# Kernel tuning notes

Hardware: AMD Instinct MI355X
Metric: run time of the kernel (lower is better)

## Reference

```python
import jax, jax.numpy as jnp
import numpy as np

# Haar (db1) filters after the index reversals done in create_wavelet_filter.
_S = np.float32(1.0 / np.sqrt(2.0))
_LO = np.array([_S, _S], np.float32)
_HI = np.array([_S, -_S], np.float32)
# dec[k, i, j]; band order: LL, (hi rows)*lo, lo*(hi cols), HH -> matches torch stack order
_DEC = np.stack([np.outer(_LO, _LO), np.outer(_HI, _LO), np.outer(_LO, _HI), np.outer(_HI, _HI)], 0)
_REC = _DEC  # identical for Haar


def dwt(x):
    # non-overlapping 2x2 stride-2 depthwise conv == blocked einsum
    b, c, h, w = x.shape
    xr = x.reshape(b, c, h // 2, 2, w // 2, 2)
    return jnp.einsum('bcipjq,kpq->bckij', xr, jnp.asarray(_DEC))  # [b,c,4,h/2,w/2]


def idwt(x):
    # stride-2 kernel-2 transposed depthwise conv == blocked einsum
    b, c, _, h, w = x.shape
    y = jnp.einsum('bckij,kpq->bcipjq', x, jnp.asarray(_REC))
    return y.reshape(b, c, 2 * h, 2 * w)


def dwconv3(x, w, bias=None):
    # depthwise 3x3 'same' conv; w: [C,1,3,3]
    c = x.shape[1]
    y = jax.lax.conv_general_dilated(x, w, (1, 1), 'SAME', feature_group_count=c,
                                     dimension_numbers=('NCHW', 'OIHW', 'NCHW'))
    if bias is not None:
        y = y + bias[None, :, None, None]
    return y


def setup_inputs() -> dict:
    key = jax.random.key(0)
    ks = jax.random.split(key, 8)
    B, C, H, W = 16, 64, 256, 256
    inp = {
        'x': jax.random.normal(ks[0], (B, C, H, W), jnp.float32),
        'base_w': jax.random.normal(ks[1], (C, 1, 3, 3), jnp.float32) * 0.1,
        'base_b': jax.random.normal(ks[2], (C,), jnp.float32) * 0.01,
        'base_scale': jnp.ones((1, C, 1, 1), jnp.float32),
        'ww0': jax.random.normal(ks[3], (4 * C, 1, 3, 3), jnp.float32) * 0.1,
        'ww1': jax.random.normal(ks[4], (4 * C, 1, 3, 3), jnp.float32) * 0.1,
        'ww2': jax.random.normal(ks[5], (4 * C, 1, 3, 3), jnp.float32) * 0.1,
        'ws0': jnp.full((1, 4 * C, 1, 1), 0.1, jnp.float32),
        'ws1': jnp.full((1, 4 * C, 1, 1), 0.1, jnp.float32),
        'ws2': jnp.full((1, 4 * C, 1, 1), 0.1, jnp.float32),
        'gamma': jnp.ones((C,), jnp.float32),
        'beta': jnp.zeros((C,), jnp.float32),
    }
    return inp


def reference(x, base_w, base_b, base_scale, ww0, ww1, ww2, ws0, ws1, ws2, gamma, beta):
    wws = [ww0, ww1, ww2]
    wss = [ws0, ws1, ws2]
    levels = 3
    lls, hs = [], []
    cur = x
    # --- WTConv2d: recursive wavelet pyramid (H,W divisible by 2**levels, no odd-pad) ---
    for i in range(levels):
        cx = dwt(cur)                # [b,c,4,h/2,w/2]
        cur = cx[:, :, 0]            # LL feeds next level
        b_, c_, _, h_, w_ = cx.shape
        t = cx.reshape(b_, c_ * 4, h_, w_)
        t = dwconv3(t, wws[i]) * wss[i]   # depthwise conv (no bias) + learned scale
        t = t.reshape(b_, c_, 4, h_, w_)
        lls.append(t[:, :, 0])
        hs.append(t[:, :, 1:4])
    nxt = jnp.zeros_like(lls[-1])
    for i in range(levels - 1, -1, -1):
        ll = lls[i] + nxt
        cx = jnp.concatenate([ll[:, :, None], hs[i]], axis=2)
        nxt = idwt(cx)
    # base depthwise conv path
    y = dwconv3(x, base_w, base_b) * base_scale + nxt
    # --- BatchNorm2d (training-mode batch stats, eps=1e-5) + ReLU ---
    mean = y.mean(axis=(0, 2, 3), keepdims=True)
    var = ((y - mean) ** 2).mean(axis=(0, 2, 3), keepdims=True)
    y = (y - mean) * jax.lax.rsqrt(var + 1e-5)
    y = y * gamma[None, :, None, None] + beta[None, :, None, None]
    return jax.nn.relu(y)
```

## Files before the change

### kernel.cpp

```cpp
#include <hip/hip_runtime.h>
#include <hip/hip_bf16.h>

#define NB 16
#define NC 64

static __device__ __forceinline__ float bfr2f(unsigned short h) {
    union { unsigned u; float f; } cv; cv.u = ((unsigned)h) << 16;
    return cv.f;
}
static __device__ __forceinline__ unsigned cvt_pk_bf16(float lo, float hi) {
    unsigned r;
    asm("v_cvt_pk_bf16_f32 %0, %1, %2" : "=v"(r) : "v"(lo), "v"(hi));
    return r;
}

template <int H>
static __device__ __forceinline__ void stage_tile(
    const float* __restrict__ src, size_t ibase, int sTop, int sLeft,
    float (*sIn)[76], int tid)
{
#pragma unroll
    for (int i = 0; i < 5; ++i) {
        int idx = i * 256 + tid;
        if (idx < 68 * 16) {
            int r = idx >> 4, c4 = (idx & 15) << 2;
            int gy = sTop + r, gx = sLeft + c4;
            float4 v = make_float4(0.f, 0.f, 0.f, 0.f);
            if ((unsigned)gy < (unsigned)H && (unsigned)gx < (unsigned)H)
                v = *(const float4*)(src + ibase + (size_t)gy * H + gx);
            *(float4*)(&sIn[r][c4]) = v;
        }
    }
    if (tid < 136) {
        int r = tid >> 1, c4 = 64 + ((tid & 1) << 2);
        int gy = sTop + r, gx = sLeft + c4;
        float4 v = make_float4(0.f, 0.f, 0.f, 0.f);
        if ((unsigned)gy < (unsigned)H && (unsigned)gx < (unsigned)H)
            v = *(const float4*)(src + ibase + (size_t)gy * H + gx);
        *(float4*)(&sIn[r][c4]) = v;
    }
}

template <int H2>
static __device__ __forceinline__ void dwt_conv_body(
    const float (*sIn)[76], const float* __restrict__ ww,
    const float* __restrict__ wsc, unsigned short* __restrict__ t_out,
    float* __restrict__ curn, int c, int b, int oy0, int ox0, int tid)
{
    const int qi = 2 * (tid >> 4), qj = 2 * (tid & 15);

    float w[4][9], sc[4];
#pragma unroll
    for (int k = 0; k < 4; ++k) {
#pragma unroll
        for (int i = 0; i < 9; ++i) w[k][i] = ww[(c * 4 + k) * 9 + i];
        sc[k] = 0.5f * wsc[c * 4 + k];
    }

    float kk[4][4];
#pragma unroll
    for (int i = 0; i < 4; ++i)
#pragma unroll
        for (int j = 0; j < 4; ++j) kk[i][j] = 0.f;
    float llc[4];

    const int pr0 = 2 * qi, pc0 = 2 * qj + 2;
#pragma unroll
    for (int rp = 0; rp < 4; ++rp) {
        float xa[8], xb[8];
#pragma unroll
        for (int n = 0; n < 4; ++n) {
            float2 va = *(const float2*)&sIn[pr0 + 2 * rp][pc0 + 2 * n];
            float2 vb = *(const float2*)&sIn[pr0 + 2 * rp + 1][pc0 + 2 * n];
            xa[2 * n] = va.x; xa[2 * n + 1] = va.y;
            xb[2 * n] = vb.x; xb[2 * n + 1] = vb.y;
        }
        float D0[4], D1[4], D2[4], D3[4];
#pragma unroll
        for (int n = 0; n < 4; ++n) {
            float a = xa[2 * n], e = xa[2 * n + 1];
            float f = xb[2 * n], g = xb[2 * n + 1];
            float s0 = a + e, s1 = f + g, d0 = a - e, d1 = f - g;
            D0[n] = s0 + s1; D1[n] = s0 - s1;
            D2[n] = d0 + d1; D3[n] = d0 - d1;
        }
#pragma unroll
        for (int mi = 0; mi < 2; ++mi) {
            const int r = rp - mi;
            if (r >= 0 && r <= 2) {
#pragma unroll
                for (int mj = 0; mj < 2; ++mj) {
                    const int m = 2 * mi + mj;
#pragma unroll
                    for (int s = 0; s < 3; ++s) {
                        kk[0][m] = fmaf(w[0][3 * r + s], D0[mj + s], kk[0][m]);
                        kk[1][m] = fmaf(w[1][3 * r + s], D1[mj + s], kk[1][m]);
                        kk[2][m] = fmaf(w[2][3 * r + s], D2[mj + s], kk[2][m]);
                        kk[3][m] = fmaf(w[3][3 * r + s], D3[mj + s], kk[3][m]);
                    }
                }
                if (r == 1) {
                    llc[2 * mi + 0] = 0.5f * D0[1];
                    llc[2 * mi + 1] = 0.5f * D0[2];
                }
            }
        }
    }

    const size_t tbase = (size_t)(b * NC + c) * 4 * H2 * H2;
    const size_t o00 = (size_t)(oy0 + qi) * H2 + (ox0 + qj);
#pragma unroll
    for (int band = 0; band < 4; ++band) {
        size_t bo = tbase + (size_t)band * H2 * H2 + o00;
#pragma unroll
        for (int mi = 0; mi < 2; ++mi)
            *(unsigned*)(t_out + bo + (size_t)mi * H2) =
                cvt_pk_bf16(kk[band][2 * mi] * sc[band], kk[band][2 * mi + 1] * sc[band]);
    }
    if (curn) {
        const size_t cbase = (size_t)(b * NC + c) * H2 * H2 + o00;
        *(float2*)(curn + cbase)      = make_float2(llc[0], llc[1]);
        *(float2*)(curn + cbase + H2) = make_float2(llc[2], llc[3]);
    }
}

__global__ __launch_bounds__(256) void dwt_conv_from_x_kernel(
    const float* __restrict__ x, const float* __restrict__ ww,
    const float* __restrict__ wsc, unsigned short* __restrict__ t_out,
    float* __restrict__ curn)
{
    const int tile = blockIdx.x;
    const int c = blockIdx.y, b = blockIdx.z;
    const int ty = tile >> 1, tx = tile & 1;
    const int oy0 = ty * 32, ox0 = tx * 32;
    const int tid = threadIdx.x;

    __shared__ float sLL[68][76];

    const size_t xbase = (size_t)(b * NC + c) * 65536;
    const int gy0 = 4 * oy0 - 4;
    const int gx0 = 4 * ox0 - 8;
    for (int u = tid; u < 68 * 36; u += 256) {
        int r = u / 36, cp = u - r * 36;
        int gy = gy0 + 2 * r, gx = gx0 + 4 * cp;
        float4 va = make_float4(0.f, 0.f, 0.f, 0.f);
        float4 vb = va;
        if ((unsigned)gy < 256u && (unsigned)gx < 256u) {
            va = *(const float4*)(x + xbase + (size_t)gy * 256 + gx);
            vb = *(const float4*)(x + xbase + (size_t)(gy + 1) * 256 + gx);
        }
        *(float2*)(&sLL[r][2 * cp]) =
            make_float2(0.5f * (va.x + va.y + vb.x + vb.y),
                        0.5f * (va.z + va.w + vb.z + vb.w));
    }
    __syncthreads();

    dwt_conv_body<64>(sLL, ww, wsc, t_out, curn, c, b, oy0, ox0, tid);
}

__global__ __launch_bounds__(256) void dwt_conv_kernel64(
    const float* __restrict__ in, const float* __restrict__ ww,
    const float* __restrict__ wsc, unsigned short* __restrict__ t_out)
{
    const int c = blockIdx.y, b = blockIdx.z;
    const int tid = threadIdx.x;
    __shared__ float sIn[68][76];
    const size_t ibase = (size_t)(b * NC + c) * 64 * 64;
    stage_tile<64>(in, ibase, -2, -4, sIn, tid);
    __syncthreads();
    dwt_conv_body<32>(sIn, ww, wsc, t_out, nullptr, c, b, 0, 0, tid);
}

__global__ __launch_bounds__(256) void idwt_fuse_kernel(
    const unsigned short* __restrict__ t1, const unsigned short* __restrict__ t2,
    unsigned short* __restrict__ nxt1)
{
    int idx = blockIdx.x * 256 + threadIdx.x;
    int j = idx & 63, i = (idx >> 6) & 63, img = idx >> 12;
    size_t t2b = (size_t)img * 4096 + (size_t)(i >> 1) * 32 + (j >> 1);
    float m0 = bfr2f(t2[t2b]);
    float m1 = bfr2f(t2[t2b + 1024]);
    float m2 = bfr2f(t2[t2b + 2048]);
    float m3 = bfr2f(t2[t2b + 3072]);
    float a1 = (i & 1) ? -m1 : m1;
    float a2 = (j & 1) ? -m2 : m2;
    float a3 = ((i ^ j) & 1) ? -m3 : m3;
    float nxt2v = 0.5f * (m0 + a1 + a2 + a3);
    size_t t1b = (size_t)img * 16384 + (size_t)i * 64 + j;
    float k0 = bfr2f(t1[t1b]) + nxt2v;
    float k1 = bfr2f(t1[t1b + 4096]);
    float k2 = bfr2f(t1[t1b + 8192]);
    float k3 = bfr2f(t1[t1b + 12288]);
    size_t ob = (size_t)img * 16384 + (size_t)(2 * i) * 128 + 2 * j;
    *(unsigned*)(nxt1 + ob)       = cvt_pk_bf16(0.5f * (k0 + k1 + k2 + k3),
                                                0.5f * (k0 + k1 - k2 - k3));
    *(unsigned*)(nxt1 + ob + 128) = cvt_pk_bf16(0.5f * (k0 - k1 + k2 - k3),
                                                0.5f * (k0 - k1 - k2 + k3));
}

__global__ __launch_bounds__(256) void final_fuse_kernel(
    const float* __restrict__ x, const unsigned short* __restrict__ nxt1,
    const float* __restrict__ bw, const float* __restrict__ bb,
    const float* __restrict__ bs, const float* __restrict__ ww0,
    const float* __restrict__ ws0,
    unsigned short* __restrict__ ybf, float2* __restrict__ partials)
{
    const int tile = blockIdx.x, c = blockIdx.y, b = blockIdx.z;
    const int ty = tile >> 2, tx = tile & 3;
    const int oy0 = ty * 64, ox0 = tx * 64;
    const int hy0 = ty * 32, hx0 = tx * 32;
    const int tid = threadIdx.x;
    const int qj = tid & 31;
    const int pr = tid >> 5;

    __shared__ float sIn[68][76];
    __shared__ float2 sW4[4];

    float w[4][9], sc[4], wb[9];
#pragma unroll
    for (int k = 0; k < 4; ++k) {
#pragma unroll
        for (int i = 0; i < 9; ++i) w[k][i] = ww0[(c * 4 + k) * 9 + i];
        sc[k] = 0.25f * ws0[c * 4 + k];
    }
#pragma unroll
    for (int i = 0; i < 9; ++i) wb[i] = bw[c * 9 + i];
    const float scale = bs[c];
    const float bsc = bb[c] * scale;

    const size_t xb = (size_t)(b * NC + c) * 65536;
    stage_tile<256>(x, xb, oy0 - 2, ox0 - 4, sIn, tid);
    __syncthreads();

    const size_t n1b = (size_t)(b * NC + c) * 16384;
    float lsum = 0.f, lss = 0.f;

#pragma unroll
    for (int pass = 0; pass < 2; ++pass) {
        const int pair = pr + 8 * pass;
        const int h0 = 2 * pair;
        const int prow0 = 4 * pair;
        const int pc0 = 2 * qj + 2;

        float kkA[4], kkB[4];
#pragma unroll
        for (int k = 0; k < 4; ++k) { kkA[k] = 0.f; kkB[k] = 0.f; }
        float acc[4][2];
#pragma unroll
        for (int p = 0; p < 4; ++p) { acc[p][0] = 0.f; acc[p][1] = 0.f; }

#pragma unroll
        for (int rp = 0; rp < 4; ++rp) {
            float xa[6], xv[6];
#pragma unroll
            for (int n = 0; n < 3; ++n) {
                float2 va = *(const float2*)&sIn[prow0 + 2 * rp][pc0 + 2 * n];
                float2 vb = *(const float2*)&sIn[prow0 + 2 * rp + 1][pc0 + 2 * n];
                xa[2 * n] = va.x; xa[2 * n + 1] = va.y;
                xv[2 * n] = vb.x; xv[2 * n + 1] = vb.y;
            }
            float D0[3], D1[3], D2[3], D3[3];
#pragma unroll
            for (int n = 0; n < 3; ++n) {
                float a = xa[2 * n], e = xa[2 * n + 1];
                float f = xv[2 * n], g = xv[2 * n + 1];
                float s0 = a + e, s1 = f + g, d0 = a - e, d1 = f - g;
                D0[n] = s0 + s1; D1[n] = s0 - s1;
                D2[n] = d0 + d1; D3[n] = d0 - d1;
            }
            if (rp <= 2) {
#pragma unroll
                for (int s = 0; s < 3; ++s) {
                    kkA[0] = fmaf(w[0][3 * rp + s], D0[s], kkA[0]);
                    kkA[1] = fmaf(w[1][3 * rp + s], D1[s], kkA[1]);
                    kkA[2] = fmaf(w[2][3 * rp + s], D2[s], kkA[2]);
                    kkA[3] = fmaf(w[3][3 * rp + s], D3[s], kkA[3]);
                }
            }
            if (rp >= 1) {
                const int r = rp - 1;
#pragma unroll
                for (int s = 0; s < 3; ++s) {
                    kkB[0] = fmaf(w[0][3 * r + s], D0[s], kkB[0]);
                    kkB[1] = fmaf(w[1][3 * r + s], D1[s], kkB[1]);
                    kkB[2] = fmaf(w[2][3 * r + s], D2[s], kkB[2]);
                    kkB[3] = fmaf(w[3][3 * r + s], D3[s], kkB[3]);
                }
            }
#pragma unroll
            for (int py = 0; py < 4; ++py) {
                const int rra = 2 * rp - py - 1;
                if (rra >= 0 && rra <= 2) {
#pragma unroll
                    for (int u = 0; u < 2; ++u)
                        acc[py][u] = fmaf(xa[u + 1], wb[3 * rra],
                                     fmaf(xa[u + 2], wb[3 * rra + 1],
                                     fmaf(xa[u + 3], wb[3 * rra + 2], acc[py][u])));
                }
                const int rrb = 2 * rp - py;
                if (rrb >= 0 && rrb <= 2) {
#pragma unroll
                    for (int u = 0; u < 2; ++u)
                        acc[py][u] = fmaf(xv[u + 1], wb[3 * rrb],
                                     fmaf(xv[u + 2], wb[3 * rrb + 1],
                                     fmaf(xv[u + 3], wb[3 * rrb + 2], acc[py][u])));
                }
            }
        }

        const float n1A = bfr2f(nxt1[n1b + (size_t)(hy0 + h0) * 128 + (hx0 + qj)]);
        const float n1B = bfr2f(nxt1[n1b + (size_t)(hy0 + h0 + 1) * 128 + (hx0 + qj)]);
        const size_t ybase = xb + (size_t)(oy0 + 4 * pair) * 256 + (ox0 + 2 * qj);
#pragma unroll
        for (int quad = 0; quad < 2; ++quad) {
            const float* kk = quad ? kkB : kkA;
            float c0 = fmaf(kk[0], sc[0], 0.5f * (quad ? n1B : n1A));
            float c1 = kk[1] * sc[1];
            float c2 = kk[2] * sc[2];
            float c3 = kk[3] * sc[3];
            float vv00 = c0 + c1 + c2 + c3;
            float vv01 = c0 + c1 - c2 - c3;
            float vv10 = c0 - c1 + c2 - c3;
            float vv11 = c0 - c1 - c2 + c3;
            float v00 = fmaf(acc[2 * quad][0],     scale, bsc) + vv00;
            float v01 = fmaf(acc[2 * quad][1],     scale, bsc) + vv01;
            float v10 = fmaf(acc[2 * quad + 1][0], scale, bsc) + vv10;
            float v11 = fmaf(acc[2 * quad + 1][1], scale, bsc) + vv11;
            lsum += v00 + v01 + v10 + v11;
            lss = fmaf(v00, v00, lss); lss = fmaf(v01, v01, lss);
            lss = fmaf(v10, v10, lss); lss = fmaf(v11, v11, lss);
            *(unsigned*)(ybf + ybase + (size_t)(2 * quad) * 256)     = cvt_pk_bf16(v00, v01);
            *(unsigned*)(ybf + ybase + (size_t)(2 * quad + 1) * 256) = cvt_pk_bf16(v10, v11);
        }
    }

#pragma unroll
    for (int off = 32; off > 0; off >>= 1) {
        lsum += __shfl_xor(lsum, off);
        lss  += __shfl_xor(lss, off);
    }
    if ((tid & 63) == 0) sW4[tid >> 6] = make_float2(lsum, lss);
    __syncthreads();
    if (tid == 0) {
        float s = sW4[0].x + sW4[1].x + sW4[2].x + sW4[3].x;
        float q = sW4[0].y + sW4[1].y + sW4[2].y + sW4[3].y;
        partials[c * 256 + b * 16 + tile] = make_float2(s, q);
    }
}

__global__ __launch_bounds__(256) void stats_kernel(
    const float2* __restrict__ partials, const float* __restrict__ gamma,
    const float* __restrict__ beta, float2* __restrict__ ab)
{
    const int c = blockIdx.x;
    const int tid = threadIdx.x;
    __shared__ float s1[256], s2[256];
    float2 p = partials[c * 256 + tid];
    s1[tid] = p.x;
    s2[tid] = p.y;
    __syncthreads();
    for (int off = 128; off > 0; off >>= 1) {
        if (tid < off) { s1[tid] += s1[tid + off]; s2[tid] += s2[tid + off]; }
        __syncthreads();
    }
    if (tid == 0) {
        const float N = (float)NB * 65536.0f;
        float mean = s1[0] / N;
        float var = s2[0] / N - mean * mean;
        float inv = rsqrtf(var + 1e-5f);
        float a = gamma[c] * inv;
        ab[c] = make_float2(a, beta[c] - mean * a);
    }
}

__global__ __launch_bounds__(256) void norm_out_kernel(
    const unsigned short* __restrict__ ybf, const float2* __restrict__ ab,
    float* __restrict__ out)
{
    const long total8 = (long)NB * NC * 65536 / 8;
    const long stride = (long)gridDim.x * 256;
    for (long i = blockIdx.x * 256L + threadIdx.x; i < total8; i += stride) {
        long e = i * 8;
        int c = (int)((e >> 16) & (NC - 1));
        float2 s = ab[c];
        uint4 v = *(const uint4*)(ybf + e);
        float4 o0, o1;
        o0.x = fmaxf(fmaf(bfr2f((unsigned short)(v.x & 0xffff)), s.x, s.y), 0.f);
        o0.y = fmaxf(fmaf(bfr2f((unsigned short)(v.x >> 16)),    s.x, s.y), 0.f);
        o0.z = fmaxf(fmaf(bfr2f((unsigned short)(v.y & 0xffff)), s.x, s.y), 0.f);
        o0.w = fmaxf(fmaf(bfr2f((unsigned short)(v.y >> 16)),    s.x, s.y), 0.f);
        o1.x = fmaxf(fmaf(bfr2f((unsigned short)(v.z & 0xffff)), s.x, s.y), 0.f);
        o1.y = fmaxf(fmaf(bfr2f((unsigned short)(v.z >> 16)),    s.x, s.y), 0.f);
        o1.z = fmaxf(fmaf(bfr2f((unsigned short)(v.w & 0xffff)), s.x, s.y), 0.f);
        o1.w = fmaxf(fmaf(bfr2f((unsigned short)(v.w >> 16)),    s.x, s.y), 0.f);
        *(float4*)(out + e) = o0;
        *(float4*)(out + e + 4) = o1;
    }
}

extern "C" void kernel_launch(void* const* d_in, const int* in_sizes, int n_in,
                              void* d_out, int out_size, void* d_ws, size_t ws_size,
                              hipStream_t stream)
{
    const float* x    = (const float*)d_in[0];
    const float* bw   = (const float*)d_in[1];
    const float* bb   = (const float*)d_in[2];
    const float* bs   = (const float*)d_in[3];
    const float* ww0  = (const float*)d_in[4];
    const float* ww1  = (const float*)d_in[5];
    const float* ww2  = (const float*)d_in[6];
    const float* ws0  = (const float*)d_in[7];
    const float* ws1  = (const float*)d_in[8];
    const float* ws2  = (const float*)d_in[9];
    const float* gamma = (const float*)d_in[10];
    const float* beta  = (const float*)d_in[11];

    char* w = (char*)d_ws;
    unsigned short* ybf  = (unsigned short*)(w);
    unsigned short* t1   = (unsigned short*)(w + 134217728);
    float*          cur2 = (float*)(w + 167772160);
    unsigned short* t2   = (unsigned short*)(w + 184549376);
    unsigned short* nxt1 = (unsigned short*)(w + 192937984);
    float2*         partials = (float2*)(w + 226492416);
    float2*         ab       = (float2*)(w + 226623488);

    dwt_conv_from_x_kernel<<<dim3(4, NC, NB), 256, 0, stream>>>(x, ww1, ws1, t1, cur2);
    dwt_conv_kernel64<<<dim3(1, NC, NB), 256, 0, stream>>>(cur2, ww2, ws2, t2);
    idwt_fuse_kernel<<<dim3(NB * NC * 4096 / 256), 256, 0, stream>>>(t1, t2, nxt1);
    final_fuse_kernel<<<dim3(16, NC, NB), 256, 0, stream>>>(x, nxt1, bw, bb, bs, ww0, ws0, ybf, partials);
    stats_kernel<<<dim3(64), 256, 0, stream>>>(partials, gamma, beta, ab);
    norm_out_kernel<<<dim3(2048), 256, 0, stream>>>(ybf, ab, (float*)d_out);
}
```

Measured before the change: 316.7 us.

## Fuse level-2 DWT conv with IDWT reconstruction and prefetch nxt1 earlier

Merges the level-2 wavelet conv kernel and the separate IDWT fuse kernel into one kernel that keeps the level-2 conv results in registers and reconstructs nxt1 directly, with vectorized t1 loads and uint4 stores. This removes one kernel launch and the t2 round trip through global memory. The shared-memory row pitch also shrinks from 76 to 72, and final_fuse now loads its nxt1 values before the barrier so their latency overlaps with staging. The fused kernel runs only 1024 blocks, and each one does more serial work than the old elementwise IDWT kernel did, so less parallelism is available.

```diff
diff --git a/kernel.cpp b/kernel.cpp
--- a/kernel.cpp
+++ b/kernel.cpp
@@ -17,7 +17,7 @@
 template <int H>
 static __device__ __forceinline__ void stage_tile(
     const float* __restrict__ src, size_t ibase, int sTop, int sLeft,
-    float (*sIn)[76], int tid)
+    float (*sIn)[72], int tid)
 {
 #pragma unroll
     for (int i = 0; i < 5; ++i) {
@@ -41,28 +41,14 @@
     }
 }
 
-template <int H2>
-static __device__ __forceinline__ void dwt_conv_body(
-    const float (*sIn)[76], const float* __restrict__ ww,
-    const float* __restrict__ wsc, unsigned short* __restrict__ t_out,
-    float* __restrict__ curn, int c, int b, int oy0, int ox0, int tid)
-{
-    const int qi = 2 * (tid >> 4), qj = 2 * (tid & 15);
-
-    float w[4][9], sc[4];
-#pragma unroll
-    for (int k = 0; k < 4; ++k) {
-#pragma unroll
-        for (int i = 0; i < 9; ++i) w[k][i] = ww[(c * 4 + k) * 9 + i];
-        sc[k] = 0.5f * wsc[c * 4 + k];
-    }
-
-    float kk[4][4];
+static __device__ __forceinline__ void dwt_conv_compute(
+    const float (*sIn)[72], const float w[4][9], float kk[4][4], float llc[4],
+    int qi, int qj)
+{
 #pragma unroll
     for (int i = 0; i < 4; ++i)
 #pragma unroll
         for (int j = 0; j < 4; ++j) kk[i][j] = 0.f;
-    float llc[4];
 
     const int pr0 = 2 * qi, pc0 = 2 * qj + 2;
 #pragma unroll
@@ -106,22 +92,6 @@
             }
         }
     }
-
-    const size_t tbase = (size_t)(b * NC + c) * 4 * H2 * H2;
-    const size_t o00 = (size_t)(oy0 + qi) * H2 + (ox0 + qj);
-#pragma unroll
-    for (int band = 0; band < 4; ++band) {
-        size_t bo = tbase + (size_t)band * H2 * H2 + o00;
-#pragma unroll
-        for (int mi = 0; mi < 2; ++mi)
-            *(unsigned*)(t_out + bo + (size_t)mi * H2) =
-                cvt_pk_bf16(kk[band][2 * mi] * sc[band], kk[band][2 * mi + 1] * sc[band]);
-    }
-    if (curn) {
-        const size_t cbase = (size_t)(b * NC + c) * H2 * H2 + o00;
-        *(float2*)(curn + cbase)      = make_float2(llc[0], llc[1]);
-        *(float2*)(curn + cbase + H2) = make_float2(llc[2], llc[3]);
-    }
 }
 
 __global__ __launch_bounds__(256) void dwt_conv_from_x_kernel(
@@ -134,8 +104,17 @@
     const int ty = tile >> 1, tx = tile & 1;
     const int oy0 = ty * 32, ox0 = tx * 32;
     const int tid = threadIdx.x;
-
-    __shared__ float sLL[68][76];
+    const int qi = 2 * (tid >> 4), qj = 2 * (tid & 15);
+
+    __shared__ float sLL[68][72];
+
+    float w[4][9], sc[4];
+#pragma unroll
+    for (int k = 0; k < 4; ++k) {
+#pragma unroll
+        for (int i = 0; i < 9; ++i) w[k][i] = ww[(c * 4 + k) * 9 + i];
+        sc[k] = 0.5f * wsc[c * 4 + k];
+    }
 
     const size_t xbase = (size_t)(b * NC + c) * 65536;
     const int gy0 = 4 * oy0 - 4;
@@ -155,47 +134,97 @@
     }
     __syncthreads();
 
-    dwt_conv_body<64>(sLL, ww, wsc, t_out, curn, c, b, oy0, ox0, tid);
-}
-
-__global__ __launch_bounds__(256) void dwt_conv_kernel64(
-    const float* __restrict__ in, const float* __restrict__ ww,
-    const float* __restrict__ wsc, unsigned short* __restrict__ t_out)
+    float kk[4][4], llc[4];
+    dwt_conv_compute(sLL, w, kk, llc, qi, qj);
+
+    const size_t tbase = (size_t)(b * NC + c) * 4 * 4096;
+    const size_t o00 = (size_t)(oy0 + qi) * 64 + (ox0 + qj);
+#pragma unroll
+    for (int band = 0; band < 4; ++band) {
+        size_t bo = tbase + (size_t)band * 4096 + o00;
+#pragma unroll
+        for (int mi = 0; mi < 2; ++mi)
+            *(unsigned*)(t_out + bo + (size_t)mi * 64) =
+                cvt_pk_bf16(kk[band][2 * mi] * sc[band], kk[band][2 * mi + 1] * sc[band]);
+    }
+    const size_t cbase = (size_t)(b * NC + c) * 4096 + o00;
+    *(float2*)(curn + cbase)      = make_float2(llc[0], llc[1]);
+    *(float2*)(curn + cbase + 64) = make_float2(llc[2], llc[3]);
+}
+
+__global__ __launch_bounds__(256) void level2_recon_kernel(
+    const float* __restrict__ cur2, const float* __restrict__ ww,
+    const float* __restrict__ wsc, const unsigned short* __restrict__ t1,
+    unsigned short* __restrict__ nxt1)
 {
     const int c = blockIdx.y, b = blockIdx.z;
     const int tid = threadIdx.x;
-    __shared__ float sIn[68][76];
-    const size_t ibase = (size_t)(b * NC + c) * 64 * 64;
-    stage_tile<64>(in, ibase, -2, -4, sIn, tid);
+    const int qi = 2 * (tid >> 4), qj = 2 * (tid & 15);
+
+    __shared__ float sIn[68][72];
+
+    float w[4][9], sc[4];
+#pragma unroll
+    for (int k = 0; k < 4; ++k) {
+#pragma unroll
+        for (int i = 0; i < 9; ++i) w[k][i] = ww[(c * 4 + k) * 9 + i];
+        sc[k] = 0.5f * wsc[c * 4 + k];
+    }
+
+    const size_t ibase = (size_t)(b * NC + c) * 4096;
+    stage_tile<64>(cur2, ibase, -2, -4, sIn, tid);
     __syncthreads();
-    dwt_conv_body<32>(sIn, ww, wsc, t_out, nullptr, c, b, 0, 0, tid);
-}
-
-__global__ __launch_bounds__(256) void idwt_fuse_kernel(
-    const unsigned short* __restrict__ t1, const unsigned short* __restrict__ t2,
-    unsigned short* __restrict__ nxt1)
-{
-    int idx = blockIdx.x * 256 + threadIdx.x;
-    int j = idx & 63, i = (idx >> 6) & 63, img = idx >> 12;
-    size_t t2b = (size_t)img * 4096 + (size_t)(i >> 1) * 32 + (j >> 1);
-    float m0 = bfr2f(t2[t2b]);
-    float m1 = bfr2f(t2[t2b + 1024]);
-    float m2 = bfr2f(t2[t2b + 2048]);
-    float m3 = bfr2f(t2[t2b + 3072]);
-    float a1 = (i & 1) ? -m1 : m1;
-    float a2 = (j & 1) ? -m2 : m2;
-    float a3 = ((i ^ j) & 1) ? -m3 : m3;
-    float nxt2v = 0.5f * (m0 + a1 + a2 + a3);
-    size_t t1b = (size_t)img * 16384 + (size_t)i * 64 + j;
-    float k0 = bfr2f(t1[t1b]) + nxt2v;
-    float k1 = bfr2f(t1[t1b + 4096]);
-    float k2 = bfr2f(t1[t1b + 8192]);
-    float k3 = bfr2f(t1[t1b + 12288]);
-    size_t ob = (size_t)img * 16384 + (size_t)(2 * i) * 128 + 2 * j;
-    *(unsigned*)(nxt1 + ob)       = cvt_pk_bf16(0.5f * (k0 + k1 + k2 + k3),
-                                                0.5f * (k0 + k1 - k2 - k3));
-    *(unsigned*)(nxt1 + ob + 128) = cvt_pk_bf16(0.5f * (k0 - k1 + k2 - k3),
-                                                0.5f * (k0 - k1 - k2 + k3));
+
+    float kk[4][4], llc[4];
+    dwt_conv_compute(sIn, w, kk, llc, qi, qj);
+#pragma unroll
+    for (int band = 0; band < 4; ++band)
+#pragma unroll
+        for (int m = 0; m < 4; ++m) kk[band][m] *= sc[band];
+
+    const size_t img = (size_t)(b * NC + c);
+    const unsigned short* t1p = t1 + img * 16384;
+    unsigned short* n1p = nxt1 + img * 16384;
+#pragma unroll
+    for (int di = 0; di < 4; ++di) {
+        const int i1 = 2 * qi + di;
+        const int col = 2 * qj;
+        uint2 r0 = *(const uint2*)(t1p +              (size_t)i1 * 64 + col);
+        uint2 r1 = *(const uint2*)(t1p + 4096 +  (size_t)i1 * 64 + col);
+        uint2 r2 = *(const uint2*)(t1p + 8192 +  (size_t)i1 * 64 + col);
+        uint2 r3 = *(const uint2*)(t1p + 12288 + (size_t)i1 * 64 + col);
+        float v0[4] = { bfr2f((unsigned short)(r0.x & 0xffff)), bfr2f((unsigned short)(r0.x >> 16)),
+                        bfr2f((unsigned short)(r0.y & 0xffff)), bfr2f((unsigned short)(r0.y >> 16)) };
+        float v1[4] = { bfr2f((unsigned short)(r1.x & 0xffff)), bfr2f((unsigned short)(r1.x >> 16)),
+                        bfr2f((unsigned short)(r1.y & 0xffff)), bfr2f((unsigned short)(r1.y >> 16)) };
+        float v2[4] = { bfr2f((unsigned short)(r2.x & 0xffff)), bfr2f((unsigned short)(r2.x >> 16)),
+                        bfr2f((unsigned short)(r2.y & 0xffff)), bfr2f((unsigned short)(r2.y >> 16)) };
+        float v3[4] = { bfr2f((unsigned short)(r3.x & 0xffff)), bfr2f((unsigned short)(r3.x >> 16)),
+                        bfr2f((unsigned short)(r3.y & 0xffff)), bfr2f((unsigned short)(r3.y >> 16)) };
+        float top[8], bot[8];
+#pragma unroll
+        for (int dj = 0; dj < 4; ++dj) {
+            const int m = 2 * (di >> 1) + (dj >> 1);
+            float m0 = kk[0][m], m1 = kk[1][m], m2 = kk[2][m], m3 = kk[3][m];
+            float s1v = (di & 1) ? -m1 : m1;
+            float s2v = (dj & 1) ? -m2 : m2;
+            float s3v = ((di ^ dj) & 1) ? -m3 : m3;
+            float k0 = v0[dj] + 0.5f * (m0 + s1v + s2v + s3v);
+            float k1 = v1[dj], k2 = v2[dj], k3 = v3[dj];
+            top[2 * dj]     = 0.5f * (k0 + k1 + k2 + k3);
+            top[2 * dj + 1] = 0.5f * (k0 + k1 - k2 - k3);
+            bot[2 * dj]     = 0.5f * (k0 - k1 + k2 - k3);
+            bot[2 * dj + 1] = 0.5f * (k0 - k1 - k2 + k3);
+        }
+        const size_t ob = (size_t)(4 * qi + 2 * di) * 128 + 4 * qj;
+        uint4 tv, bv;
+        tv.x = cvt_pk_bf16(top[0], top[1]); tv.y = cvt_pk_bf16(top[2], top[3]);
+        tv.z = cvt_pk_bf16(top[4], top[5]); tv.w = cvt_pk_bf16(top[6], top[7]);
+        bv.x = cvt_pk_bf16(bot[0], bot[1]); bv.y = cvt_pk_bf16(bot[2], bot[3]);
+        bv.z = cvt_pk_bf16(bot[4], bot[5]); bv.w = cvt_pk_bf16(bot[6], bot[7]);
+        *(uint4*)(n1p + ob) = tv;
+        *(uint4*)(n1p + ob + 128) = bv;
+    }
 }
 
 __global__ __launch_bounds__(256) void final_fuse_kernel(
@@ -213,7 +242,7 @@
     const int qj = tid & 31;
     const int pr = tid >> 5;
 
-    __shared__ float sIn[68][76];
+    __shared__ float sIn[68][72];
     __shared__ float2 sW4[4];
 
     float w[4][9], sc[4], wb[9];
@@ -230,15 +259,20 @@
 
     const size_t xb = (size_t)(b * NC + c) * 65536;
     stage_tile<256>(x, xb, oy0 - 2, ox0 - 4, sIn, tid);
+
+    const size_t n1b = (size_t)(b * NC + c) * 16384 + hx0 + qj;
+    const float n1p0A = bfr2f(nxt1[n1b + (size_t)(hy0 + 2 * pr) * 128]);
+    const float n1p0B = bfr2f(nxt1[n1b + (size_t)(hy0 + 2 * pr + 1) * 128]);
+    const float n1p1A = bfr2f(nxt1[n1b + (size_t)(hy0 + 2 * pr + 16) * 128]);
+    const float n1p1B = bfr2f(nxt1[n1b + (size_t)(hy0 + 2 * pr + 17) * 128]);
+
     __syncthreads();
 
-    const size_t n1b = (size_t)(b * NC + c) * 16384;
     float lsum = 0.f, lss = 0.f;
 
 #pragma unroll
     for (int pass = 0; pass < 2; ++pass) {
         const int pair = pr + 8 * pass;
-        const int h0 = 2 * pair;
         const int prow0 = 4 * pair;
         const int pc0 = 2 * qj + 2;
 
@@ -308,8 +342,8 @@
             }
         }
 
-        const float n1A = bfr2f(nxt1[n1b + (size_t)(hy0 + h0) * 128 + (hx0 + qj)]);
-        const float n1B = bfr2f(nxt1[n1b + (size_t)(hy0 + h0 + 1) * 128 + (hx0 + qj)]);
+        const float n1A = pass ? n1p1A : n1p0A;
+        const float n1B = pass ? n1p1B : n1p0B;
         const size_t ybase = xb + (size_t)(oy0 + 4 * pair) * 256 + (ox0 + 2 * qj);
 #pragma unroll
         for (int quad = 0; quad < 2; ++quad) {
@@ -419,14 +453,12 @@
     unsigned short* ybf  = (unsigned short*)(w);
     unsigned short* t1   = (unsigned short*)(w + 134217728);
     float*          cur2 = (float*)(w + 167772160);
-    unsigned short* t2   = (unsigned short*)(w + 184549376);
-    unsigned short* nxt1 = (unsigned short*)(w + 192937984);
-    float2*         partials = (float2*)(w + 226492416);
-    float2*         ab       = (float2*)(w + 226623488);
+    unsigned short* nxt1 = (unsigned short*)(w + 184549376);
+    float2*         partials = (float2*)(w + 218103808);
+    float2*         ab       = (float2*)(w + 218234880);
 
     dwt_conv_from_x_kernel<<<dim3(4, NC, NB), 256, 0, stream>>>(x, ww1, ws1, t1, cur2);
-    dwt_conv_kernel64<<<dim3(1, NC, NB), 256, 0, stream>>>(cur2, ww2, ws2, t2);
-    idwt_fuse_kernel<<<dim3(NB * NC * 4096 / 256), 256, 0, stream>>>(t1, t2, nxt1);
+    level2_recon_kernel<<<dim3(1, NC, NB), 256, 0, stream>>>(cur2, ww2, ws2, t1, nxt1);
     final_fuse_kernel<<<dim3(16, NC, NB), 256, 0, stream>>>(x, nxt1, bw, bb, bs, ww0, ws0, ybf, partials);
     stats_kernel<<<dim3(64), 256, 0, stream>>>(partials, gamma, beta, ab);
     norm_out_kernel<<<dim3(2048), 256, 0, stream>>>(ybf, ab, (float*)d_out);
```

Result: faster. 301.8 us (-4.7%).
